# Performance work log

Hardware: AMD Instinct MI355X
Metric: run time of the kernel (lower is better)

## Reference

```python
import jax, jax.numpy as jnp
import numpy as np

NUM_HEADS = 16
DIM_K = 128
DIM_V = 128
ROPE_BASE = 10000.0


def rope(x):
    # x: [..., seq, d]; rotate-half convention
    d = x.shape[-1]
    seq = x.shape[-2]
    half = d // 2
    inv_freq = 1.0 / (ROPE_BASE ** (jnp.arange(0, half, dtype=jnp.float32) / half))
    ang = jnp.arange(seq, dtype=jnp.float32)[:, None] * inv_freq[None, :]  # [seq, half]
    cos, sin = jnp.cos(ang), jnp.sin(ang)
    x1, x2 = x[..., :half], x[..., half:]
    return jnp.concatenate([x1 * cos - x2 * sin, x1 * sin + x2 * cos], axis=-1)


def setup_inputs() -> dict:
    key = jax.random.key(0)
    ks = jax.random.split(key, 8)
    B, S, D = 2, 2048, 2048
    s = lambda fan_in: 1.0 / np.sqrt(fan_in)
    return {
        'q_in': jax.random.normal(ks[0], (B, S, D), jnp.float32),
        'k_in': jax.random.normal(ks[1], (B, S, D), jnp.float32),
        'v_in': jax.random.normal(ks[2], (B, S, D), jnp.float32),
        'mask': jnp.zeros((B, S), dtype=bool),
        'Wq': jax.random.normal(ks[3], (D, NUM_HEADS * DIM_K), jnp.float32) * s(D),
        'bq': jnp.zeros((NUM_HEADS * DIM_K,), jnp.float32),
        'Wk': jax.random.normal(ks[4], (D, DIM_K), jnp.float32) * s(D),
        'bk': jnp.zeros((DIM_K,), jnp.float32),
        'Wv': jax.random.normal(ks[5], (D, DIM_V), jnp.float32) * s(D),
        'bv': jnp.zeros((DIM_V,), jnp.float32),
        'Wo': jax.random.normal(ks[6], (NUM_HEADS * DIM_V, D), jnp.float32) * s(NUM_HEADS * DIM_V),
        'bo': jnp.zeros((D,), jnp.float32),
    }


def reference(q_in, k_in, v_in, mask, Wq, bq, Wk, bk, Wv, bv, Wo, bo):
    B, Sq, _ = q_in.shape
    Sk = k_in.shape[1]
    # projections: multi-head Q, single shared K/V head (MQA)
    q = (q_in @ Wq + bq).reshape(B, Sq, NUM_HEADS, DIM_K).transpose(0, 2, 1, 3)  # [B,H,Sq,dk]
    k = k_in @ Wk + bk  # [B,Sk,dk]
    v = v_in @ Wv + bv  # [B,Sk,dv]
    # inline RoPE on q and k
    q = rope(q)
    k = rope(k)
    scores = jnp.einsum('bhqd,bkd->bhqk', q, k) / np.sqrt(DIM_K)  # [B,H,Sq,Sk]
    # padding mask: True means masked out
    scores = jnp.where(mask[:, None, None, :], -jnp.inf, scores)
    # causal mask
    causal = jnp.triu(jnp.ones((Sq, Sk), dtype=bool), k=1)
    scores = jnp.where(causal[None, None], -jnp.inf, scores)
    weights = jax.nn.softmax(scores, axis=-1)
    attn = jnp.einsum('bhqk,bkd->bhqd', weights, v)  # [B,H,Sq,dv]
    attn = attn.transpose(0, 2, 1, 3).reshape(B, Sq, NUM_HEADS * DIM_V)
    return attn @ Wo + bo
```

## Files before the change

### kernel.cpp

```cpp
#include <hip/hip_runtime.h>

#define NHEADS 16
#define DKV 128
#define BB 2
#define SS 2048
#define DD 2048

typedef __attribute__((ext_vector_type(8))) short bf16x8;
typedef __attribute__((ext_vector_type(4))) short bf16x4;
typedef __attribute__((ext_vector_type(4))) float f32x4;
typedef __attribute__((ext_vector_type(8))) _Float16 f16x8;

#define QSCL 0.12752775f

__device__ __forceinline__ short f2bf(float x) {
  unsigned u = __builtin_bit_cast(unsigned, x);
  unsigned r = (u + 0x7fffu + ((u >> 16) & 1u)) >> 16;
  return (short)(unsigned short)r;
}
__device__ __forceinline__ float bf2f(short s) {
  unsigned u = ((unsigned)(unsigned short)s) << 16;
  return __builtin_bit_cast(float, u);
}
__device__ __forceinline__ unsigned pk2bf(float a, float b) {
#if __has_builtin(__builtin_amdgcn_cvt_pk_bf16_f32)
  typedef __attribute__((ext_vector_type(2))) __bf16 bf2_t;
  bf2_t r = __builtin_amdgcn_cvt_pk_bf16_f32(a, b);
  return __builtin_bit_cast(unsigned, r);
#else
  unsigned ua = __builtin_bit_cast(unsigned, a);
  unsigned ub = __builtin_bit_cast(unsigned, b);
  return ((ua + 0x8000u) >> 16) | ((ub + 0x8000u) & 0xffff0000u);
#endif
}
__device__ __forceinline__ unsigned pkf16(float a, float b) {
#if __has_builtin(__builtin_amdgcn_cvt_pkrtz)
  typedef __attribute__((ext_vector_type(2))) __fp16 h2_t;
  h2_t r = __builtin_amdgcn_cvt_pkrtz(a, b);
  return __builtin_bit_cast(unsigned, r);
#else
  _Float16 ha = (_Float16)a, hb = (_Float16)b;
  unsigned short ua = __builtin_bit_cast(unsigned short, ha);
  unsigned short ub = __builtin_bit_cast(unsigned short, hb);
  return (unsigned)ua | ((unsigned)ub << 16);
#endif
}
__device__ __forceinline__ float exp2fast(float x) {
#if __has_builtin(__builtin_amdgcn_exp2f)
  return __builtin_amdgcn_exp2f(x);
#else
  return exp2f(x);
#endif
}

__device__ __forceinline__ void async16(const void* g, void* l) {
  __builtin_amdgcn_global_load_lds(
      (__attribute__((address_space(1))) void*)g,
      (__attribute__((address_space(3))) void*)l, 16, 0, 0);
}

__global__ __launch_bounds__(256) void cvt_q(const float* __restrict__ x,
                                             short* __restrict__ y) {
  int idx = blockIdx.x * 256 + threadIdx.x;
  int g = idx * 8;
  float4 a = *(const float4*)(x + g);
  float4 b = *(const float4*)(x + g + 4);
  uint4 o = {pk2bf(a.x, a.y), pk2bf(a.z, a.w), pk2bf(b.x, b.y), pk2bf(b.z, b.w)};
  *(uint4*)(y + g) = o;
}

__global__ __launch_bounds__(256) void transpose_w(
    const float* __restrict__ W, short* __restrict__ Wt, int K, int N,
    float scale) {
  __shared__ float T[32][33];
  const int nt = blockIdx.x * 32;
  const int kt = blockIdx.y * 32;
  const int tx = threadIdx.x & 31;
  const int ty = threadIdx.x >> 5;
#pragma unroll
  for (int i = 0; i < 4; ++i)
    T[ty + i * 8][tx] = W[(size_t)(kt + ty + i * 8) * N + nt + tx];
  __syncthreads();
#pragma unroll
  for (int i = 0; i < 4; ++i)
    Wt[(size_t)(nt + ty + i * 8) * K + kt + tx] = f2bf(T[tx][ty + i * 8] * scale);
}

__global__ void mask_bias(const unsigned char* __restrict__ m,
                          float* __restrict__ mb) {
  int i = blockIdx.x * 256 + threadIdx.x;
  mb[i] = m[i] ? -1e30f : 0.0f;
}

template <int AMODE>
__global__ __launch_bounds__(256) void gemm_as(
    const void* __restrict__ Ap, const short* __restrict__ Bt,
    const float* __restrict__ bias, void* __restrict__ Cp,
    int M, int N, int K, int KC, int cmode, float bscale) {
  __shared__ __align__(16) short As[128 * 32];
  __shared__ __align__(16) short Bs[128 * 32];
  const int tid = threadIdx.x;
  const int bm = blockIdx.y * 128;
  const int bn = blockIdx.x * 128;
  const int kz = blockIdx.z;
  const int w = tid >> 6, lane = tid & 63;
  const int lm = lane & 15, q4 = lane >> 4;
  const int m0 = (w & 1) * 64, n0 = (w >> 1) * 64;

  f32x4 acc[4][4];
#pragma unroll
  for (int mi = 0; mi < 4; ++mi)
#pragma unroll
    for (int ni = 0; ni < 4; ++ni) acc[mi][ni] = (f32x4){0.f, 0.f, 0.f, 0.f};

  const int kbeg = kz * KC;
  const int kend = kbeg + KC;

  for (int k0 = kbeg; k0 < kend; k0 += 32) {
    __syncthreads();
    if (AMODE == 1) {
      const short* Ab = (const short*)Ap;
#pragma unroll
      for (int i = 0; i < 2; ++i) {
        int rA = (w * 2 + i) * 16 + (lane >> 2);
        int cA = (lane & 3) ^ (rA & 3);
        async16(Ab + (size_t)(bm + rA) * K + k0 + cA * 8, &As[(w * 2 + i) * 512]);
      }
    } else {
      const float* Af = (const float*)Ap;
      float4 av[4];
#pragma unroll
      for (int i = 0; i < 4; ++i) {
        int qd = tid + i * 256;
        int r = qd >> 3, cq = qd & 7;
        av[i] = *(const float4*)(Af + (size_t)(bm + r) * K + k0 + cq * 4);
      }
#pragma unroll
      for (int i = 0; i < 4; ++i) {
        int qd = tid + i * 256;
        int r = qd >> 3, cq = qd & 7;
        int ch = cq >> 1, hf = cq & 1;
        int pc = ch ^ (r & 3);
        bf16x4 t = {f2bf(av[i].x), f2bf(av[i].y), f2bf(av[i].z), f2bf(av[i].w)};
        *(bf16x4*)&As[r * 32 + pc * 8 + hf * 4] = t;
      }
    }
#pragma unroll
    for (int i = 0; i < 2; ++i) {
      int rB = (w * 2 + i) * 16 + (lane >> 2);
      int cB = (lane & 3) ^ (rB & 3);
      async16(Bt + (size_t)(bn + rB) * K + k0 + cB * 8, &Bs[(w * 2 + i) * 512]);
    }
    __syncthreads();

    bf16x8 af[4], bf[4];
#pragma unroll
    for (int mi = 0; mi < 4; ++mi)
      af[mi] = *(const bf16x8*)&As[(m0 + mi * 16 + lm) * 32 + ((q4 ^ (lm & 3)) * 8)];
#pragma unroll
    for (int ni = 0; ni < 4; ++ni)
      bf[ni] = *(const bf16x8*)&Bs[(n0 + ni * 16 + lm) * 32 + ((q4 ^ (lm & 3)) * 8)];
#pragma unroll
    for (int mi = 0; mi < 4; ++mi)
#pragma unroll
      for (int ni = 0; ni < 4; ++ni)
        acc[mi][ni] = __builtin_amdgcn_mfma_f32_16x16x32_bf16(
            af[mi], bf[ni], acc[mi][ni], 0, 0, 0);
  }

  if (cmode == 2) {
    float* Cf = (float*)Cp + (size_t)kz * M * N;
#pragma unroll
    for (int mi = 0; mi < 4; ++mi)
#pragma unroll
      for (int ni = 0; ni < 4; ++ni)
#pragma unroll
        for (int reg = 0; reg < 4; ++reg)
          Cf[(size_t)(bm + m0 + mi * 16 + q4 * 4 + reg) * N +
             (bn + n0 + ni * 16 + lm)] = acc[mi][ni][reg];
  } else {
#pragma unroll
    for (int mi = 0; mi < 4; ++mi)
#pragma unroll
      for (int ni = 0; ni < 4; ++ni)
#pragma unroll
        for (int reg = 0; reg < 4; ++reg) {
          int rowg = bm + m0 + mi * 16 + q4 * 4 + reg;
          int colg = bn + n0 + ni * 16 + lm;
          float val = acc[mi][ni][reg] + bias[colg] * bscale;
          if (cmode == 0)
            ((float*)Cp)[(size_t)rowg * N + colg] = val;
          else
            ((short*)Cp)[(size_t)rowg * N + colg] = f2bf(val);
        }
  }
}

#define SPLITK 4
__global__ __launch_bounds__(256) void kv_reduce(
    const float* __restrict__ kpart, const float* __restrict__ vpart,
    const float* __restrict__ bk, const float* __restrict__ bv,
    short* __restrict__ kp, short* __restrict__ vtb) {
  __shared__ float Kt[32][128];
  __shared__ short Vl[128][36];
  const int tid = threadIdx.x;
  const int r0 = blockIdx.x * 32;
#pragma unroll
  for (int i = 0; i < 16; ++i) {
    int e = tid + i * 256;
    int r = e >> 7, c = e & 127;
    float sk = 0.f, sv = 0.f;
#pragma unroll
    for (int z = 0; z < SPLITK; ++z) {
      sk += kpart[((size_t)z * 4096 + r0 + r) * 128 + c];
      sv += vpart[((size_t)z * 4096 + r0 + r) * 128 + c];
    }
    Kt[r][c] = sk + bk[c];
    Vl[c][r] = f2bf(sv + bv[c]);
  }
  __syncthreads();
#pragma unroll
  for (int i = 0; i < 8; ++i) {
    int e = tid + i * 256;
    int r = e >> 6, d = e & 63;
    float x1 = Kt[r][d], x2 = Kt[r][d + 64];
    float s = (float)((r0 + r) & (SS - 1));
    float ang = s * exp2fast((float)d * (-13.287712379549449f / 64.0f));
    float sn, cs;
    __sincosf(ang, &sn, &cs);
    kp[(size_t)(r0 + r) * 128 + d] = f2bf(x1 * cs - x2 * sn);
    kp[(size_t)(r0 + r) * 128 + d + 64] = f2bf(x1 * sn + x2 * cs);
  }
  const int b = r0 >> 11;
  const int j = tid >> 1, soff = (tid & 1) * 16;
  short* dst = vtb + ((size_t)b * 128 + j) * SS + (r0 & (SS - 1)) + soff;
#pragma unroll
  for (int t = 0; t < 2; ++t) {
    bf16x8 tmp;
#pragma unroll
    for (int u = 0; u < 8; ++u) tmp[u] = Vl[j][soff + t * 8 + u];
    *(bf16x8*)(dst + t * 8) = tmp;
  }
}

__global__ __launch_bounds__(256) void rope_q(short* __restrict__ qp) {
  int idx = blockIdx.x * 256 + threadIdx.x;
  int j8 = idx & 7;
  int h = (idx >> 3) & (NHEADS - 1);
  int s = (idx >> 7) & (SS - 1);
  int b = idx >> 18;
  short* base = qp + (((size_t)b * SS + s) * NHEADS + h) * DKV + j8 * 8;
  bf16x8 x1 = *(bf16x8*)base;
  bf16x8 x2 = *(bf16x8*)(base + 64);
  bf16x8 y1, y2;
#pragma unroll
  for (int j = 0; j < 8; ++j) {
    int d = j8 * 8 + j;
    float ang = (float)s * exp2fast((float)d * (-13.287712379549449f / 64.0f));
    float sn, cs;
    __sincosf(ang, &sn, &cs);
    float a = bf2f(x1[j]), bb2 = bf2f(x2[j]);
    y1[j] = f2bf(a * cs - bb2 * sn);
    y2[j] = f2bf(a * sn + bb2 * cs);
  }
  *(bf16x8*)base = y1;
  *(bf16x8*)(base + 64) = y2;
}

#define PSTR 40

__global__ __launch_bounds__(256, 2) void flash_kernel(
    const short* __restrict__ q, const short* __restrict__ k,
    const short* __restrict__ vt, const float* __restrict__ mb,
    short* __restrict__ out, short* __restrict__ pO, float* __restrict__ pL) {
  __shared__ __align__(16) short Kb[2][32 * 128];
  __shared__ __align__(16) short Vb[2][128 * 64];
  __shared__ __align__(16) short Ps[4][32 * PSTR];
  const int j = blockIdx.x;
  const int cls = j >> 5, hb = j & 31;
  int qx, c;
  if (cls < 8) {
    qx = cls + 8; c = 0;
  } else {
    int kk = (cls - 8) >> 1;
    if ((cls & 1) == 0) { qx = 15 - kk; c = 1; }
    else                { qx = 7 - kk;  c = 0; }
  }
  const int h = hb & 15, b = hb >> 4;
  const int kt0 = c ? 32 : 0;
  int kend = 4 * qx + 4;
  if (c == 0 && kend > 32) kend = 32;

  const int tid = threadIdx.x;
  const int w = tid >> 6, lane = tid & 63;
  const int lm = lane & 15, q4 = lane >> 4;
  const int qrow0 = qx * 128 + w * 32;

  bf16x8 qf[2][4];
#pragma unroll
  for (int ni = 0; ni < 2; ++ni)
#pragma unroll
    for (int ks = 0; ks < 4; ++ks)
      qf[ni][ks] = *(const bf16x8*)(q +
          ((size_t)b * SS + qrow0 + ni * 16 + lm) * (NHEADS * DKV) + h * DKV +
          ks * 32 + q4 * 8);

  bf16x8 onesb;
#pragma unroll
  for (int jj = 0; jj < 8; ++jj) onesb[jj] = (short)0x3F80;

  f32x4 O[8][2], Ol[2];
#pragma unroll
  for (int vi = 0; vi < 8; ++vi)
#pragma unroll
    for (int ni = 0; ni < 2; ++ni) O[vi][ni] = (f32x4){0.f, 0.f, 0.f, 0.f};
#pragma unroll
  for (int ni = 0; ni < 2; ++ni) Ol[ni] = (f32x4){0.f, 0.f, 0.f, 0.f};

  const size_t kbase = (size_t)b * SS;

  {
#pragma unroll
    for (int i = 0; i < 2; ++i) {
      int r = (w * 2 + i) * 4 + (lane >> 4);
      int cc = (lane & 15) ^ (r & 7);
      async16(k + (kbase + (size_t)kt0 * 32 + r) * DKV + cc * 8,
              &Kb[0][(w * 2 + i) * 512]);
    }
#pragma unroll
    for (int i = 0; i < 4; ++i) {
      int rV = (w * 4 + i) * 8 + (lane >> 3);
      int cV = (lane & 7) ^ (rV & 7);
      async16(vt + ((size_t)b * DKV + rV) * SS + (size_t)kt0 * 32 + cV * 8,
              &Vb[0][(w * 4 + i) * 512]);
    }
  }
  f32x4 mc0 = *(const f32x4*)(mb + kbase + (size_t)kt0 * 32 + q4 * 4);
  f32x4 mc1 = *(const f32x4*)(mb + kbase + (size_t)kt0 * 32 + 16 + q4 * 4);

  for (int kt = kt0; kt < kend; ++kt) {
    __syncthreads();

    f32x4 mn0, mn1;
    if (kt + 1 < kend) {
      const int t = kt + 1;
#pragma unroll
      for (int i = 0; i < 2; ++i) {
        int r = (w * 2 + i) * 4 + (lane >> 4);
        int cc = (lane & 15) ^ (r & 7);
        async16(k + (kbase + (size_t)t * 32 + r) * DKV + cc * 8,
                &Kb[t & 1][(w * 2 + i) * 512]);
      }
      if (kt & 1) {
#pragma unroll
        for (int i = 0; i < 4; ++i) {
          int rV = (w * 4 + i) * 8 + (lane >> 3);
          int cV = (lane & 7) ^ (rV & 7);
          async16(vt + ((size_t)b * DKV + rV) * SS + (size_t)t * 32 + cV * 8,
                  &Vb[(t >> 1) & 1][(w * 4 + i) * 512]);
        }
      }
      mn0 = *(const f32x4*)(mb + kbase + (size_t)t * 32 + q4 * 4);
      mn1 = *(const f32x4*)(mb + kbase + (size_t)t * 32 + 16 + q4 * 4);
    }

    const short* Kc = Kb[kt & 1];
    f32x4 sacc[2][2];
#pragma unroll
    for (int mi = 0; mi < 2; ++mi)
#pragma unroll
      for (int ni = 0; ni < 2; ++ni) sacc[mi][ni] = (f32x4){0.f, 0.f, 0.f, 0.f};
#pragma unroll
    for (int mi = 0; mi < 2; ++mi)
#pragma unroll
      for (int ks = 0; ks < 4; ++ks) {
        bf16x8 kf = *(const bf16x8*)&Kc[(mi * 16 + lm) * 128 +
                                        (((ks * 4 + q4) ^ (lm & 7)) << 3)];
#pragma unroll
        for (int ni = 0; ni < 2; ++ni)
          sacc[mi][ni] = __builtin_amdgcn_mfma_f32_16x16x32_bf16(
              kf, qf[ni][ks], sacc[mi][ni], 0, 0, 0);
      }

    const bool diag = (kt >= 4 * qx);
#pragma unroll
    for (int mi = 0; mi < 2; ++mi) {
      f32x4 mbv = mi ? mc1 : mc0;
#pragma unroll
      for (int ni = 0; ni < 2; ++ni) {
        float pv[4];
#pragma unroll
        for (int reg = 0; reg < 4; ++reg) {
          float s = sacc[mi][ni][reg] + mbv[reg];
          if (diag) {
            int kg = kt * 32 + mi * 16 + q4 * 4 + reg;
            int qg = qrow0 + ni * 16 + lm;
            if (kg > qg) s = -1e30f;
          }
          pv[reg] = exp2fast(s);
        }
        uint2 pkd = {pk2bf(pv[0], pv[1]), pk2bf(pv[2], pv[3])};
        *(uint2*)&Ps[w][(ni * 16 + lm) * PSTR + mi * 16 + q4 * 4] = pkd;
      }
    }
    mc0 = mn0;
    mc1 = mn1;

    const short* Vc = Vb[(kt >> 1) & 1];
    const int hf4 = (kt & 1) * 4;
    bf16x8 pf[2];
#pragma unroll
    for (int ni = 0; ni < 2; ++ni) {
      pf[ni] = *(const bf16x8*)&Ps[w][(ni * 16 + lm) * PSTR + q4 * 8];
      Ol[ni] = __builtin_amdgcn_mfma_f32_16x16x32_bf16(pf[ni], onesb, Ol[ni], 0, 0, 0);
    }
#pragma unroll
    for (int vi = 0; vi < 8; ++vi) {
      bf16x8 vf = *(const bf16x8*)&Vc[(vi * 16 + lm) * 64 +
                                      (((hf4 + q4) ^ (lm & 7)) << 3)];
#pragma unroll
      for (int ni = 0; ni < 2; ++ni)
        O[vi][ni] = __builtin_amdgcn_mfma_f32_16x16x32_bf16(
            pf[ni], vf, O[vi][ni], 0, 0, 0);
    }
  }

  __syncthreads();
  float* Wr = (float*)&Vb[0][0] + w * 2048;
  float linv[2][4];
#pragma unroll
  for (int ni = 0; ni < 2; ++ni)
#pragma unroll
    for (int reg = 0; reg < 4; ++reg) linv[ni][reg] = 1.0f / Ol[ni][reg];

  const bool split = (qx >= 8);
  short* obase;
  int ostr;
  if (split) {
    int slot = ((b * 16 + h) * 8 + (qx - 8)) * 2 + c;
    obase = pO + (size_t)slot * (128 * 128);
    ostr = 128;
    if (lm == 0) {
      float* dl = pL + (size_t)slot * 128 + w * 32;
#pragma unroll
      for (int ni = 0; ni < 2; ++ni)
#pragma unroll
        for (int reg = 0; reg < 4; ++reg)
          dl[ni * 16 + q4 * 4 + reg] = Ol[ni][reg];
    }
  } else {
    obase = out + ((size_t)b * SS + qx * 128) * (NHEADS * DKV) + h * DKV;
    ostr = NHEADS * DKV;
  }

#pragma unroll
  for (int qd = 0; qd < 4; ++qd) {
#pragma unroll
    for (int v2 = 0; v2 < 2; ++v2) {
      int vi = qd * 2 + v2;
#pragma unroll
      for (int ni = 0; ni < 2; ++ni)
#pragma unroll
        for (int reg = 0; reg < 4; ++reg)
          Wr[(ni * 16 + q4 * 4 + reg) * 34 + v2 * 16 + lm] =
              O[vi][ni][reg] * linv[ni][reg];
    }
    int r = lane & 31, hh = lane >> 5;
    f32x4 t0 = *(const f32x4*)&Wr[r * 34 + hh * 16];
    f32x4 t1 = *(const f32x4*)&Wr[r * 34 + hh * 16 + 4];
    f32x4 t2 = *(const f32x4*)&Wr[r * 34 + hh * 16 + 8];
    f32x4 t3 = *(const f32x4*)&Wr[r * 34 + hh * 16 + 12];
    size_t oaddr = (size_t)(w * 32 + r) * ostr + qd * 32 + hh * 16;
    uint4 o0, o1;
    if (split) {
      o0 = (uint4){pkf16(t0[0], t0[1]), pkf16(t0[2], t0[3]),
                   pkf16(t1[0], t1[1]), pkf16(t1[2], t1[3])};
      o1 = (uint4){pkf16(t2[0], t2[1]), pkf16(t2[2], t2[3]),
                   pkf16(t3[0], t3[1]), pkf16(t3[2], t3[3])};
    } else {
      o0 = (uint4){pk2bf(t0[0], t0[1]), pk2bf(t0[2], t0[3]),
                   pk2bf(t1[0], t1[1]), pk2bf(t1[2], t1[3])};
      o1 = (uint4){pk2bf(t2[0], t2[1]), pk2bf(t2[2], t2[3]),
                   pk2bf(t3[0], t3[1]), pk2bf(t3[2], t3[3])};
    }
    *(uint4*)(obase + oaddr) = o0;
    *(uint4*)(obase + oaddr + 8) = o1;
  }
}

__global__ __launch_bounds__(256) void combine(
    const short* __restrict__ pO, const float* __restrict__ pL,
    short* __restrict__ out) {
  const int qxi = blockIdx.x, h = blockIdx.y, b = blockIdx.z;
  const int qx = 8 + qxi;
  const int slot2 = ((b * 16 + h) * 8 + qxi) * 2;
  const _Float16* p0 = (const _Float16*)(pO + (size_t)slot2 * (128 * 128));
  const _Float16* p1 = p0 + 128 * 128;
  const float* l0 = pL + (size_t)slot2 * 128;
  const float* l1 = l0 + 128;
  const int t = threadIdx.x;
  const int row = t >> 1, half = t & 1;
  const float w0 = l0[row], w1 = l1[row];
  const float inv = 1.0f / (w0 + w1);
  const float a0 = w0 * inv, a1 = w1 * inv;
  const int off = row * 128 + half * 64;
  short* dst = out + ((size_t)(b * SS + qx * 128 + row)) * (NHEADS * DKV) +
               h * DKV + half * 64;
#pragma unroll
  for (int v = 0; v < 8; ++v) {
    f16x8 x0 = *(const f16x8*)(p0 + off + v * 8);
    f16x8 x1 = *(const f16x8*)(p1 + off + v * 8);
    float r[8];
#pragma unroll
    for (int u = 0; u < 8; ++u)
      r[u] = (float)x0[u] * a0 + (float)x1[u] * a1;
    uint4 o = {pk2bf(r[0], r[1]), pk2bf(r[2], r[3]),
               pk2bf(r[4], r[5]), pk2bf(r[6], r[7])};
    *(uint4*)(dst + v * 8) = o;
  }
}

extern "C" void kernel_launch(void* const* d_in, const int* in_sizes, int n_in,
                              void* d_out, int out_size, void* d_ws, size_t ws_size,
                              hipStream_t stream) {
  const float* q_in = (const float*)d_in[0];
  const float* k_in = (const float*)d_in[1];
  const float* v_in = (const float*)d_in[2];
  const unsigned char* mask = (const unsigned char*)d_in[3];
  const float* Wq = (const float*)d_in[4];
  const float* bq = (const float*)d_in[5];
  const float* Wk = (const float*)d_in[6];
  const float* bk = (const float*)d_in[7];
  const float* Wv = (const float*)d_in[8];
  const float* bv = (const float*)d_in[9];
  const float* Wo = (const float*)d_in[10];
  const float* bo = (const float*)d_in[11];

  const int M = BB * SS;
  short* Wqt = (short*)d_ws;
  short* Wot = Wqt + (size_t)DD * DD;
  short* Wkt = Wot + (size_t)DD * DD;
  short* Wvt = Wkt + (size_t)DKV * DD;
  short* qb  = Wvt + (size_t)DKV * DD;
  short* qp  = qb + (size_t)M * DD;
  short* kp  = qp + (size_t)M * DD;
  short* vtb = kp + (size_t)M * DKV;
  float* mb  = (float*)(vtb + (size_t)BB * DKV * SS);
  float* kpart = mb + (size_t)BB * SS;
  float* vpart = kpart + (size_t)SPLITK * M * DKV;
  float* pL = vpart + (size_t)SPLITK * M * DKV;
  short* ap = qb;
  short* pO = (short*)kpart;

  cvt_q<<<M * DD / (8 * 256), 256, 0, stream>>>(q_in, qb);
  transpose_w<<<dim3(DD / 32, DD / 32), 256, 0, stream>>>(Wq, Wqt, DD, DD, QSCL);
  transpose_w<<<dim3(DKV / 32, DD / 32), 256, 0, stream>>>(Wk, Wkt, DD, DKV, 1.0f);
  transpose_w<<<dim3(DKV / 32, DD / 32), 256, 0, stream>>>(Wv, Wvt, DD, DKV, 1.0f);
  transpose_w<<<dim3(DD / 32, DD / 32), 256, 0, stream>>>(Wo, Wot, DD, DD, 1.0f);
  mask_bias<<<BB * SS / 256, 256, 0, stream>>>(mask, mb);

  gemm_as<1><<<dim3(DD / 128, M / 128, 1), 256, 0, stream>>>(
      qb, Wqt, bq, qp, M, DD, DD, DD, 1, QSCL);
  gemm_as<0><<<dim3(1, M / 128, SPLITK), 256, 0, stream>>>(
      k_in, Wkt, nullptr, kpart, M, DKV, DD, DD / SPLITK, 2, 1.0f);
  gemm_as<0><<<dim3(1, M / 128, SPLITK), 256, 0, stream>>>(
      v_in, Wvt, nullptr, vpart, M, DKV, DD, DD / SPLITK, 2, 1.0f);
  kv_reduce<<<M / 32, 256, 0, stream>>>(kpart, vpart, bk, bv, kp, vtb);
  rope_q<<<(BB * SS * NHEADS * 8) / 256, 256, 0, stream>>>(qp);

  flash_kernel<<<dim3(768), 256, 0, stream>>>(qp, kp, vtb, mb, ap, pO, pL);
  combine<<<dim3(8, NHEADS, BB), 256, 0, stream>>>(pO, pL, ap);

  gemm_as<1><<<dim3(DD / 128, M / 128, 1), 256, 0, stream>>>(
      ap, Wot, bo, d_out, M, DD, DD, DD, 0, 1.0f);
}
```

Baseline: 419.4 us.

## Split flash attention block across 8 waves with 16 query rows each

The flash kernel now launches 512 threads per block, and each of 8 waves owns 16 query rows instead of 4 waves owning 32. Per-wave accumulators and Q fragments are halved, and the K/V async loads are spread over more waves. The aim is to cut register pressure and raise occupancy and latency hiding. The cost is that each K/V fragment read from shared memory now feeds fewer MFMAs, so LDS traffic per FLOP doubles.

```diff
diff --git a/kernel.cpp b/kernel.cpp
--- a/kernel.cpp
+++ b/kernel.cpp
@@ -269,13 +269,13 @@
 
 #define PSTR 40
 
-__global__ __launch_bounds__(256, 2) void flash_kernel(
+__global__ __launch_bounds__(512, 4) void flash_kernel(
     const short* __restrict__ q, const short* __restrict__ k,
     const short* __restrict__ vt, const float* __restrict__ mb,
     short* __restrict__ out, short* __restrict__ pO, float* __restrict__ pL) {
   __shared__ __align__(16) short Kb[2][32 * 128];
   __shared__ __align__(16) short Vb[2][128 * 64];
-  __shared__ __align__(16) short Ps[4][32 * PSTR];
+  __shared__ __align__(16) short Ps[8][16 * PSTR];
   const int j = blockIdx.x;
   const int cls = j >> 5, hb = j & 31;
   int qx, c;
@@ -294,45 +294,39 @@
   const int tid = threadIdx.x;
   const int w = tid >> 6, lane = tid & 63;
   const int lm = lane & 15, q4 = lane >> 4;
-  const int qrow0 = qx * 128 + w * 32;
-
-  bf16x8 qf[2][4];
-#pragma unroll
-  for (int ni = 0; ni < 2; ++ni)
-#pragma unroll
-    for (int ks = 0; ks < 4; ++ks)
-      qf[ni][ks] = *(const bf16x8*)(q +
-          ((size_t)b * SS + qrow0 + ni * 16 + lm) * (NHEADS * DKV) + h * DKV +
-          ks * 32 + q4 * 8);
+  const int qrow0 = qx * 128 + w * 16;
+
+  bf16x8 qf[4];
+#pragma unroll
+  for (int ks = 0; ks < 4; ++ks)
+    qf[ks] = *(const bf16x8*)(q +
+        ((size_t)b * SS + qrow0 + lm) * (NHEADS * DKV) + h * DKV +
+        ks * 32 + q4 * 8);
 
   bf16x8 onesb;
 #pragma unroll
   for (int jj = 0; jj < 8; ++jj) onesb[jj] = (short)0x3F80;
 
-  f32x4 O[8][2], Ol[2];
-#pragma unroll
-  for (int vi = 0; vi < 8; ++vi)
-#pragma unroll
-    for (int ni = 0; ni < 2; ++ni) O[vi][ni] = (f32x4){0.f, 0.f, 0.f, 0.f};
-#pragma unroll
-  for (int ni = 0; ni < 2; ++ni) Ol[ni] = (f32x4){0.f, 0.f, 0.f, 0.f};
+  f32x4 O[8], Ol;
+#pragma unroll
+  for (int vi = 0; vi < 8; ++vi) O[vi] = (f32x4){0.f, 0.f, 0.f, 0.f};
+  Ol = (f32x4){0.f, 0.f, 0.f, 0.f};
 
   const size_t kbase = (size_t)b * SS;
 
   {
-#pragma unroll
-    for (int i = 0; i < 2; ++i) {
-      int r = (w * 2 + i) * 4 + (lane >> 4);
+    {
+      int r = w * 4 + (lane >> 4);
       int cc = (lane & 15) ^ (r & 7);
       async16(k + (kbase + (size_t)kt0 * 32 + r) * DKV + cc * 8,
-              &Kb[0][(w * 2 + i) * 512]);
-    }
-#pragma unroll
-    for (int i = 0; i < 4; ++i) {
-      int rV = (w * 4 + i) * 8 + (lane >> 3);
+              &Kb[0][w * 512]);
+    }
+#pragma unroll
+    for (int i = 0; i < 2; ++i) {
+      int rV = (w * 2 + i) * 8 + (lane >> 3);
       int cV = (lane & 7) ^ (rV & 7);
       async16(vt + ((size_t)b * DKV + rV) * SS + (size_t)kt0 * 32 + cV * 8,
-              &Vb[0][(w * 4 + i) * 512]);
+              &Vb[0][(w * 2 + i) * 512]);
     }
   }
   f32x4 mc0 = *(const f32x4*)(mb + kbase + (size_t)kt0 * 32 + q4 * 4);
@@ -344,20 +338,19 @@
     f32x4 mn0, mn1;
     if (kt + 1 < kend) {
       const int t = kt + 1;
-#pragma unroll
-      for (int i = 0; i < 2; ++i) {
-        int r = (w * 2 + i) * 4 + (lane >> 4);
+      {
+        int r = w * 4 + (lane >> 4);
         int cc = (lane & 15) ^ (r & 7);
         async16(k + (kbase + (size_t)t * 32 + r) * DKV + cc * 8,
-                &Kb[t & 1][(w * 2 + i) * 512]);
+                &Kb[t & 1][w * 512]);
       }
       if (kt & 1) {
 #pragma unroll
-        for (int i = 0; i < 4; ++i) {
-          int rV = (w * 4 + i) * 8 + (lane >> 3);
+        for (int i = 0; i < 2; ++i) {
+          int rV = (w * 2 + i) * 8 + (lane >> 3);
           int cV = (lane & 7) ^ (rV & 7);
           async16(vt + ((size_t)b * DKV + rV) * SS + (size_t)t * 32 + cV * 8,
-                  &Vb[(t >> 1) & 1][(w * 4 + i) * 512]);
+                  &Vb[(t >> 1) & 1][(w * 2 + i) * 512]);
         }
       }
       mn0 = *(const f32x4*)(mb + kbase + (size_t)t * 32 + q4 * 4);
@@ -365,73 +358,57 @@
     }
 
     const short* Kc = Kb[kt & 1];
-    f32x4 sacc[2][2];
-#pragma unroll
-    for (int mi = 0; mi < 2; ++mi)
-#pragma unroll
-      for (int ni = 0; ni < 2; ++ni) sacc[mi][ni] = (f32x4){0.f, 0.f, 0.f, 0.f};
+    f32x4 sacc[2];
+#pragma unroll
+    for (int mi = 0; mi < 2; ++mi) sacc[mi] = (f32x4){0.f, 0.f, 0.f, 0.f};
 #pragma unroll
     for (int mi = 0; mi < 2; ++mi)
 #pragma unroll
       for (int ks = 0; ks < 4; ++ks) {
         bf16x8 kf = *(const bf16x8*)&Kc[(mi * 16 + lm) * 128 +
                                         (((ks * 4 + q4) ^ (lm & 7)) << 3)];
-#pragma unroll
-        for (int ni = 0; ni < 2; ++ni)
-          sacc[mi][ni] = __builtin_amdgcn_mfma_f32_16x16x32_bf16(
-              kf, qf[ni][ks], sacc[mi][ni], 0, 0, 0);
+        sacc[mi] = __builtin_amdgcn_mfma_f32_16x16x32_bf16(
+            kf, qf[ks], sacc[mi], 0, 0, 0);
       }
 
     const bool diag = (kt >= 4 * qx);
 #pragma unroll
     for (int mi = 0; mi < 2; ++mi) {
       f32x4 mbv = mi ? mc1 : mc0;
-#pragma unroll
-      for (int ni = 0; ni < 2; ++ni) {
-        float pv[4];
-#pragma unroll
-        for (int reg = 0; reg < 4; ++reg) {
-          float s = sacc[mi][ni][reg] + mbv[reg];
-          if (diag) {
-            int kg = kt * 32 + mi * 16 + q4 * 4 + reg;
-            int qg = qrow0 + ni * 16 + lm;
-            if (kg > qg) s = -1e30f;
-          }
-          pv[reg] = exp2fast(s);
+      float pv[4];
+#pragma unroll
+      for (int reg = 0; reg < 4; ++reg) {
+        float s = sacc[mi][reg] + mbv[reg];
+        if (diag) {
+          int kg = kt * 32 + mi * 16 + q4 * 4 + reg;
+          int qg = qrow0 + lm;
+          if (kg > qg) s = -1e30f;
         }
-        uint2 pkd = {pk2bf(pv[0], pv[1]), pk2bf(pv[2], pv[3])};
-        *(uint2*)&Ps[w][(ni * 16 + lm) * PSTR + mi * 16 + q4 * 4] = pkd;
-      }
+        pv[reg] = exp2fast(s);
+      }
+      uint2 pkd = {pk2bf(pv[0], pv[1]), pk2bf(pv[2], pv[3])};
+      *(uint2*)&Ps[w][lm * PSTR + mi * 16 + q4 * 4] = pkd;
     }
     mc0 = mn0;
     mc1 = mn1;
 
     const short* Vc = Vb[(kt >> 1) & 1];
     const int hf4 = (kt & 1) * 4;
-    bf16x8 pf[2];
-#pragma unroll
-    for (int ni = 0; ni < 2; ++ni) {
-      pf[ni] = *(const bf16x8*)&Ps[w][(ni * 16 + lm) * PSTR + q4 * 8];
-      Ol[ni] = __builtin_amdgcn_mfma_f32_16x16x32_bf16(pf[ni], onesb, Ol[ni], 0, 0, 0);
-    }
+    bf16x8 pf = *(const bf16x8*)&Ps[w][lm * PSTR + q4 * 8];
+    Ol = __builtin_amdgcn_mfma_f32_16x16x32_bf16(pf, onesb, Ol, 0, 0, 0);
 #pragma unroll
     for (int vi = 0; vi < 8; ++vi) {
       bf16x8 vf = *(const bf16x8*)&Vc[(vi * 16 + lm) * 64 +
                                       (((hf4 + q4) ^ (lm & 7)) << 3)];
-#pragma unroll
-      for (int ni = 0; ni < 2; ++ni)
-        O[vi][ni] = __builtin_amdgcn_mfma_f32_16x16x32_bf16(
-            pf[ni], vf, O[vi][ni], 0, 0, 0);
+      O[vi] = __builtin_amdgcn_mfma_f32_16x16x32_bf16(pf, vf, O[vi], 0, 0, 0);
     }
   }
 
   __syncthreads();
-  float* Wr = (float*)&Vb[0][0] + w * 2048;
-  float linv[2][4];
-#pragma unroll
-  for (int ni = 0; ni < 2; ++ni)
-#pragma unroll
-    for (int reg = 0; reg < 4; ++reg) linv[ni][reg] = 1.0f / Ol[ni][reg];
+  float* Wr = (float*)&Vb[0][0] + w * 544;
+  float linv[4];
+#pragma unroll
+  for (int reg = 0; reg < 4; ++reg) linv[reg] = 1.0f / Ol[reg];
 
   const bool split = (qx >= 8);
   short* obase;
@@ -441,12 +418,10 @@
     obase = pO + (size_t)slot * (128 * 128);
     ostr = 128;
     if (lm == 0) {
-      float* dl = pL + (size_t)slot * 128 + w * 32;
-#pragma unroll
-      for (int ni = 0; ni < 2; ++ni)
-#pragma unroll
-        for (int reg = 0; reg < 4; ++reg)
-          dl[ni * 16 + q4 * 4 + reg] = Ol[ni][reg];
+      float* dl = pL + (size_t)slot * 128 + w * 16;
+#pragma unroll
+      for (int reg = 0; reg < 4; ++reg)
+        dl[q4 * 4 + reg] = Ol[reg];
     }
   } else {
     obase = out + ((size_t)b * SS + qx * 128) * (NHEADS * DKV) + h * DKV;
@@ -459,32 +434,22 @@
     for (int v2 = 0; v2 < 2; ++v2) {
       int vi = qd * 2 + v2;
 #pragma unroll
-      for (int ni = 0; ni < 2; ++ni)
-#pragma unroll
-        for (int reg = 0; reg < 4; ++reg)
-          Wr[(ni * 16 + q4 * 4 + reg) * 34 + v2 * 16 + lm] =
-              O[vi][ni][reg] * linv[ni][reg];
-    }
-    int r = lane & 31, hh = lane >> 5;
-    f32x4 t0 = *(const f32x4*)&Wr[r * 34 + hh * 16];
-    f32x4 t1 = *(const f32x4*)&Wr[r * 34 + hh * 16 + 4];
-    f32x4 t2 = *(const f32x4*)&Wr[r * 34 + hh * 16 + 8];
-    f32x4 t3 = *(const f32x4*)&Wr[r * 34 + hh * 16 + 12];
-    size_t oaddr = (size_t)(w * 32 + r) * ostr + qd * 32 + hh * 16;
-    uint4 o0, o1;
+      for (int reg = 0; reg < 4; ++reg)
+        Wr[(q4 * 4 + reg) * 34 + v2 * 16 + lm] = O[vi][reg] * linv[reg];
+    }
+    int r = lane & 15, hh = lane >> 4;
+    f32x4 t0 = *(const f32x4*)&Wr[r * 34 + hh * 8];
+    f32x4 t1 = *(const f32x4*)&Wr[r * 34 + hh * 8 + 4];
+    size_t oaddr = (size_t)(w * 16 + r) * ostr + qd * 32 + hh * 8;
+    uint4 o0;
     if (split) {
       o0 = (uint4){pkf16(t0[0], t0[1]), pkf16(t0[2], t0[3]),
                    pkf16(t1[0], t1[1]), pkf16(t1[2], t1[3])};
-      o1 = (uint4){pkf16(t2[0], t2[1]), pkf16(t2[2], t2[3]),
-                   pkf16(t3[0], t3[1]), pkf16(t3[2], t3[3])};
     } else {
       o0 = (uint4){pk2bf(t0[0], t0[1]), pk2bf(t0[2], t0[3]),
                    pk2bf(t1[0], t1[1]), pk2bf(t1[2], t1[3])};
-      o1 = (uint4){pk2bf(t2[0], t2[1]), pk2bf(t2[2], t2[3]),
-                   pk2bf(t3[0], t3[1]), pk2bf(t3[2], t3[3])};
     }
     *(uint4*)(obase + oaddr) = o0;
-    *(uint4*)(obase + oaddr + 8) = o1;
   }
 }
 
@@ -568,7 +533,7 @@
   kv_reduce<<<M / 32, 256, 0, stream>>>(kpart, vpart, bk, bv, kp, vtb);
   rope_q<<<(BB * SS * NHEADS * 8) / 256, 256, 0, stream>>>(qp);
 
-  flash_kernel<<<dim3(768), 256, 0, stream>>>(qp, kp, vtb, mb, ap, pO, pL);
+  flash_kernel<<<dim3(768), 512, 0, stream>>>(qp, kp, vtb, mb, ap, pO, pL);
   combine<<<dim3(8, NHEADS, BB), 256, 0, stream>>>(pO, pL, ap);
 
   gemm_as<1><<<dim3(DD / 128, M / 128, 1), 256, 0, stream>>>(
```

Result: no change. 420.1 us (+0.2%).
